# Kernel tuning notes

Measured on AMD Instinct MI355X. Metric: run time of the kernel, lower is better.

Reference implementation:

```python
import jax, jax.numpy as jnp
import numpy as np

TOP_P = 0.9
NEG_FILL = -1000000000.0


def _top_p_mask(logits):
    # probabilities over vocab
    probs = jax.nn.softmax(logits, axis=-1)
    # sort descending; keep the permutation to scatter the mask back
    order = jnp.argsort(-probs, axis=-1)                      # [B, V]
    ordered = jnp.take_along_axis(probs, order, axis=-1)      # [B, V]
    cum = jnp.cumsum(ordered, axis=-1)
    cum = cum.at[..., -1].set(0.0)
    cum = jnp.roll(cum, shift=1, axis=-1)                     # exclusive cumsum
    cmask = cum <= TOP_P                                      # [B, V] in sorted order
    # scatter back: selection[b, order[b, j]] = cmask[b, j]  <=>  gather by inverse perm
    inv = jnp.argsort(order, axis=-1)
    return jnp.take_along_axis(cmask, inv, axis=-1)


def setup_inputs() -> dict:
    key = jax.random.key(0)
    k1, k2 = jax.random.split(key)
    B, V = 256, 128000
    logits = jax.random.normal(k1, (B, V), dtype=jnp.float32)
    u = jax.random.uniform(k2, (B,), dtype=jnp.float32)
    return {"logits": logits, "u": u, "temperature": 1}


def reference(logits, u, temperature):
    t = jnp.asarray(temperature, dtype=logits.dtype)
    logits = logits / t
    sel = _top_p_mask(logits)
    masked = jnp.where(sel, logits, jnp.asarray(NEG_FILL, logits.dtype))
    probs = jax.nn.softmax(masked, axis=-1)                   # [B, V]
    # multinomial(num_samples=1) via inverse-CDF with uniform u
    cdf = jnp.cumsum(probs, axis=-1)
    token = jnp.sum(cdf < u[:, None], axis=-1)
    return jnp.minimum(token, probs.shape[-1] - 1)
```

## Files before the change

### kernel.cpp

```cpp
#include <hip/hip_runtime.h>

#define BLOCK 1024
#define NW (BLOCK / 64)
#define FPSCALE 8192.0f
#define INVSCALE 0x1p-13f

__device__ __forceinline__ float wincl(float v, int lane) {
#pragma unroll
    for (int o = 1; o < 64; o <<= 1) {
        float x = __shfl_up(v, o, 64);
        if (lane >= o) v += x;
    }
    return v;
}

__device__ __forceinline__ void find_crit_desc(const float* h, int n, int seg,
                                               float limit, int lane, int* out_b) {
    float segsum = 0.f;
    int start = n - 1 - lane * seg;
    for (int k = 0; k < seg; k++) segsum += h[start - k];
    float incl = wincl(segsum, lane);
    unsigned long long mk = __ballot(incl > limit);
    if (mk == 0ULL) { *out_b = 0; return; }
    int fl = __ffsll(mk) - 1;
    float base = __shfl(incl, fl, 64) - __shfl(segsum, fl, 64);
    int sstart = n - 1 - fl * seg;
    float v = (lane < seg) ? h[sstart - lane] : 0.f;
    float incl2 = wincl(v, lane);
    unsigned long long mk2 = __ballot((lane < seg) && (base + incl2 > limit));
    int k2 = mk2 ? (__ffsll(mk2) - 1) : (seg - 1);
    *out_b = sstart - k2;
}

#define OKEY(bb) ((bb) ^ ((unsigned)((int)(bb) >> 31) | 0x80000000u))

#define LD4(j) (*(const float4*)(row + (j)))

__global__ __launch_bounds__(BLOCK) void NucleusSampling_79336635892529_kernel(
    const float* __restrict__ logits, const float* __restrict__ uvec,
    const int* __restrict__ temp, int* __restrict__ out, int Vv) {
    const int b = blockIdx.x;
    const float* __restrict__ row = logits + (size_t)b * (size_t)Vv;
    const int t = threadIdx.x;
    const int lane = t & 63;
    const int wave = t >> 6;
    const int rep = lane & 3;

    __shared__ __align__(16) unsigned histbuf[8192];
    __shared__ float mg[2048];
    __shared__ float sweep[NW];
    __shared__ float csum[128];
    __shared__ int shb1;

    const float inv_t = 1.0f / (float)temp[0];
    const int V4 = Vv & ~3;
    const int S = BLOCK * 4;
    const int nch = (Vv + 1023) >> 10;

    for (int i = t; i < 8192; i += BLOCK) histbuf[i] = 0u;
    __syncthreads();

#define P1(xx) { unsigned kk = OKEY(__float_as_uint(xx)); \
                 float e = __expf((xx) * inv_t); \
                 atomicAdd(&histbuf[((kk >> 21) << 2) | rep], \
                           (unsigned)(e * FPSCALE + 0.5f)); }
    {
        int i = t * 4;
        for (; i + 3 * S + 3 < V4; i += 4 * S) {
            float4 a = LD4(i), b4 = LD4(i + S), c = LD4(i + 2 * S), d = LD4(i + 3 * S);
            P1(a.x); P1(a.y); P1(a.z); P1(a.w);
            P1(b4.x); P1(b4.y); P1(b4.z); P1(b4.w);
            P1(c.x); P1(c.y); P1(c.z); P1(c.w);
            P1(d.x); P1(d.y); P1(d.z); P1(d.w);
        }
        for (; i < V4; i += S) { float4 a = LD4(i); P1(a.x); P1(a.y); P1(a.z); P1(a.w); }
        for (int j = V4 + t; j < Vv; j += BLOCK) P1(row[j]);
    }
    __syncthreads();

    float zp = 0.f;
    for (int i = t; i < 2048; i += BLOCK) {
        uint4 m4 = *(const uint4*)&histbuf[i << 2];
        float m = (float)(m4.x + m4.y + m4.z + m4.w) * INVSCALE;
        mg[i] = m;
        zp += m;
    }
#pragma unroll
    for (int o = 32; o >= 1; o >>= 1) zp += __shfl_xor(zp, o, 64);
    if (lane == 0) sweep[wave] = zp;
    __syncthreads();
    float Z = 0.f;
    for (int w = 0; w < NW; w++) Z += sweep[w];
    const float limit = 0.9f * Z;

    if (wave == 0) {
        int b1w;
        find_crit_desc(mg, 2048, 32, limit, lane, &b1w);
        if (lane == 0) shb1 = b1w;
    }
    if (t < 128 && t >= nch) csum[t] = 0.f;
    __syncthreads();
    const unsigned Tlow = (unsigned)shb1 << 21;

#define P2(xx, ss) { unsigned kk = OKEY(__float_as_uint(xx)); \
                     float e = __expf((xx) * inv_t); \
                     if (kk >= Tlow) ss += e; }
    for (int c0 = wave; c0 < nch; c0 += 2 * NW) {
        const int c1 = c0 + NW;
        const bool haveB = (c1 < nch);
        float s0 = 0.f, s1 = 0.f;
        const int bA = c0 << 10, bB = c1 << 10;
        if (bA + 1024 <= Vv && (!haveB || bB + 1024 <= Vv)) {
            float4 a0 = LD4(bA + lane * 4);
            float4 a1 = LD4(bA + 256 + lane * 4);
            float4 a2 = LD4(bA + 512 + lane * 4);
            float4 a3 = LD4(bA + 768 + lane * 4);
            if (haveB) {
                float4 b0 = LD4(bB + lane * 4);
                float4 b1v = LD4(bB + 256 + lane * 4);
                float4 b2 = LD4(bB + 512 + lane * 4);
                float4 b3 = LD4(bB + 768 + lane * 4);
                P2(b0.x, s1); P2(b0.y, s1); P2(b0.z, s1); P2(b0.w, s1);
                P2(b1v.x, s1); P2(b1v.y, s1); P2(b1v.z, s1); P2(b1v.w, s1);
                P2(b2.x, s1); P2(b2.y, s1); P2(b2.z, s1); P2(b2.w, s1);
                P2(b3.x, s1); P2(b3.y, s1); P2(b3.z, s1); P2(b3.w, s1);
            }
            P2(a0.x, s0); P2(a0.y, s0); P2(a0.z, s0); P2(a0.w, s0);
            P2(a1.x, s0); P2(a1.y, s0); P2(a1.z, s0); P2(a1.w, s0);
            P2(a2.x, s0); P2(a2.y, s0); P2(a2.z, s0); P2(a2.w, s0);
            P2(a3.x, s0); P2(a3.y, s0); P2(a3.z, s0); P2(a3.w, s0);
        } else {
            for (int q = 0; q < 16; q++) {
                int i = bA + (q << 6) + lane;
                if (i < Vv) { float x = row[i]; P2(x, s0); }
            }
            if (haveB) {
                for (int q = 0; q < 16; q++) {
                    int i = bB + (q << 6) + lane;
                    if (i < Vv) { float x = row[i]; P2(x, s1); }
                }
            }
        }
#pragma unroll
        for (int o = 32; o >= 1; o >>= 1) s0 += __shfl_xor(s0, o, 64);
        if (lane == 0) csum[c0] = s0;
        if (haveB) {
#pragma unroll
            for (int o = 32; o >= 1; o >>= 1) s1 += __shfl_xor(s1, o, 64);
            if (lane == 0) csum[c1] = s1;
        }
    }
    __syncthreads();

    if (wave == 0) {
        float segsum = csum[lane * 2] + csum[lane * 2 + 1];
        float incl = wincl(segsum, lane);
        float total = __shfl(incl, 63, 64);
        const float U = uvec[b] * total;
        unsigned long long mk = __ballot(incl >= U);
        int token;
        if (mk == 0ULL) {
            token = Vv;
        } else {
            int fl = __ffsll(mk) - 1;
            float base = __shfl(incl, fl, 64) - __shfl(segsum, fl, 64);
            float v = (lane < 2) ? csum[fl * 2 + lane] : 0.f;
            float incl2 = wincl(v, lane);
            unsigned long long mk2 = __ballot((lane < 2) && (base + incl2 >= U));
            int k2i = mk2 ? (__ffsll(mk2) - 1) : 1;
            int cx = fl * 2 + k2i;
            float B = base + __shfl(incl2, k2i, 64) - __shfl(v, k2i, 64);
            int cb = cx << 10;
            float vv[16];
#pragma unroll
            for (int r = 0; r < 16; r++) {
                int idx = cb + r * 64 + lane;
                vv[r] = (idx < Vv) ? row[idx] : -1e30f;
            }
            int cnt2 = 0;
#pragma unroll
            for (int r = 0; r < 16; r++) {
                int idx = cb + r * 64 + lane;
                unsigned kk = OKEY(__float_as_uint(vv[r]));
                float e = __expf(vv[r] * inv_t);
                float keep = (kk >= Tlow) ? e : 0.f;
                float is = wincl(keep, lane);
                unsigned long long mm = __ballot((idx < Vv) && (B + is < U));
                cnt2 += __popcll(mm);
                B += __shfl(is, 63, 64);
            }
            token = cb + cnt2;
        }
        if (lane == 0) out[b] = (token < Vv - 1) ? token : (Vv - 1);
    }
}

extern "C" void kernel_launch(void* const* d_in, const int* in_sizes, int n_in,
                              void* d_out, int out_size, void* d_ws, size_t ws_size,
                              hipStream_t stream) {
    const float* logits = (const float*)d_in[0];
    const float* u = (const float*)d_in[1];
    const int* temp = (const int*)d_in[2];
    int* out = (int*)d_out;
    int B = in_sizes[1];
    int V = in_sizes[0] / B;
    NucleusSampling_79336635892529_kernel<<<B, BLOCK, 0, stream>>>(logits, u, temp, out, V);
}
```

Measured before the change: 213.0 us.

## Split per-row sampling into four kernels with two blocks per row

Replaces the single fused one-block-per-row kernel with four kernels: a histogram pass that uses two blocks per row, a threshold walk, a chunk-sum pass that also uses two blocks per row, and a single-wave pick kernel. Intermediates go through the workspace. With 256 rows, the fused kernel launches only 256 blocks, and the split doubles block count to fill more of the GPU. The cost is extra launches and global-memory round trips for the partial histograms and chunk sums. If the workspace is missing or too small, the original fused kernel still runs.

```diff
diff --git a/kernel.cpp b/kernel.cpp
--- a/kernel.cpp
+++ b/kernel.cpp
@@ -36,6 +36,211 @@
 
 #define LD4(j) (*(const float4*)(row + (j)))
 
+#define P1(xx) { unsigned kk = OKEY(__float_as_uint(xx)); \
+                 float e = __expf((xx) * inv_t); \
+                 atomicAdd(&histbuf[((kk >> 21) << 2) | rep], \
+                           (unsigned)(e * FPSCALE + 0.5f)); }
+
+#define P2(xx, ss) { unsigned kk = OKEY(__float_as_uint(xx)); \
+                     float e = __expf((xx) * inv_t); \
+                     if (kk >= Tlow) ss += e; }
+
+__global__ __launch_bounds__(BLOCK, 8) void ns_hist(
+    const float* __restrict__ logits, const int* __restrict__ temp,
+    unsigned* __restrict__ part, int Vv) {
+    const int bid = blockIdx.x;
+    const int b = bid >> 1, h = bid & 1;
+    const float* __restrict__ row = logits + (size_t)b * (size_t)Vv;
+    const int t = threadIdx.x;
+    const int rep = t & 3;
+
+    __shared__ __align__(16) unsigned histbuf[8192];
+
+    const float inv_t = 1.0f / (float)temp[0];
+    const int S = BLOCK * 4;
+    const int HL = (((Vv + 1) >> 1) + 3) & ~3;
+    const int lo = h * HL;
+    const int hi = min(Vv, lo + HL);
+    const int hi4 = (hi > lo) ? lo + ((hi - lo) & ~3) : lo;
+
+    for (int i = t; i < 8192; i += BLOCK) histbuf[i] = 0u;
+    __syncthreads();
+
+    {
+        int i = lo + t * 4;
+        for (; i + 3 * S + 3 < hi4; i += 4 * S) {
+            float4 a = LD4(i), b4 = LD4(i + S), c = LD4(i + 2 * S), d = LD4(i + 3 * S);
+            P1(a.x); P1(a.y); P1(a.z); P1(a.w);
+            P1(b4.x); P1(b4.y); P1(b4.z); P1(b4.w);
+            P1(c.x); P1(c.y); P1(c.z); P1(c.w);
+            P1(d.x); P1(d.y); P1(d.z); P1(d.w);
+        }
+        for (; i + 3 < hi4; i += S) { float4 a = LD4(i); P1(a.x); P1(a.y); P1(a.z); P1(a.w); }
+        for (int j = hi4 + t; j < hi; j += BLOCK) P1(row[j]);
+    }
+    __syncthreads();
+
+    unsigned* __restrict__ dst = part + (size_t)bid * 2048;
+    for (int i = t; i < 2048; i += BLOCK) {
+        uint4 m4 = *(const uint4*)&histbuf[i << 2];
+        dst[i] = m4.x + m4.y + m4.z + m4.w;
+    }
+}
+
+__global__ __launch_bounds__(BLOCK) void ns_walk(
+    const unsigned* __restrict__ part, unsigned* __restrict__ tlow, int Bn) {
+    const int b = blockIdx.x;
+    const int t = threadIdx.x;
+    const int lane = t & 63;
+    const int wave = t >> 6;
+
+    __shared__ float mg[2048];
+    __shared__ float sweep[NW];
+
+    const unsigned* __restrict__ pa = part + (size_t)(b * 2) * 2048;
+    const unsigned* __restrict__ pb = part + (size_t)(b * 2 + 1) * 2048;
+
+    float zp = 0.f;
+    for (int i = t; i < 2048; i += BLOCK) {
+        float m = (float)(pa[i] + pb[i]) * INVSCALE;
+        mg[i] = m;
+        zp += m;
+    }
+#pragma unroll
+    for (int o = 32; o >= 1; o >>= 1) zp += __shfl_xor(zp, o, 64);
+    if (lane == 0) sweep[wave] = zp;
+    __syncthreads();
+    float Z = 0.f;
+    for (int w = 0; w < NW; w++) Z += sweep[w];
+    const float limit = 0.9f * Z;
+
+    if (wave == 0) {
+        int b1w;
+        find_crit_desc(mg, 2048, 32, limit, lane, &b1w);
+        if (lane == 0) tlow[b] = (unsigned)b1w << 21;
+    }
+}
+
+__global__ __launch_bounds__(BLOCK, 8) void ns_csum(
+    const float* __restrict__ logits, const int* __restrict__ temp,
+    const unsigned* __restrict__ tlow, float* __restrict__ csum, int Vv) {
+    const int bid = blockIdx.x;
+    const int b = bid >> 1, h = bid & 1;
+    const float* __restrict__ row = logits + (size_t)b * (size_t)Vv;
+    const int t = threadIdx.x;
+    const int lane = t & 63;
+    const int wave = t >> 6;
+
+    const float inv_t = 1.0f / (float)temp[0];
+    const unsigned Tlow = tlow[b];
+    const int nch = (Vv + 1023) >> 10;
+    const int nchh = (nch + 1) >> 1;
+    const int clo = h * nchh;
+    const int chi = min(nch, clo + nchh);
+    float* __restrict__ cs = csum + (size_t)b * 128;
+
+    for (int c0 = clo + wave; c0 < chi; c0 += 2 * NW) {
+        const int c1 = c0 + NW;
+        const bool haveB = (c1 < chi);
+        float s0 = 0.f, s1 = 0.f;
+        const int bA = c0 << 10, bB = c1 << 10;
+        if (bA + 1024 <= Vv && (!haveB || bB + 1024 <= Vv)) {
+            float4 a0 = LD4(bA + lane * 4);
+            float4 a1 = LD4(bA + 256 + lane * 4);
+            float4 a2 = LD4(bA + 512 + lane * 4);
+            float4 a3 = LD4(bA + 768 + lane * 4);
+            if (haveB) {
+                float4 b0 = LD4(bB + lane * 4);
+                float4 b1v = LD4(bB + 256 + lane * 4);
+                float4 b2 = LD4(bB + 512 + lane * 4);
+                float4 b3 = LD4(bB + 768 + lane * 4);
+                P2(b0.x, s1); P2(b0.y, s1); P2(b0.z, s1); P2(b0.w, s1);
+                P2(b1v.x, s1); P2(b1v.y, s1); P2(b1v.z, s1); P2(b1v.w, s1);
+                P2(b2.x, s1); P2(b2.y, s1); P2(b2.z, s1); P2(b2.w, s1);
+                P2(b3.x, s1); P2(b3.y, s1); P2(b3.z, s1); P2(b3.w, s1);
+            }
+            P2(a0.x, s0); P2(a0.y, s0); P2(a0.z, s0); P2(a0.w, s0);
+            P2(a1.x, s0); P2(a1.y, s0); P2(a1.z, s0); P2(a1.w, s0);
+            P2(a2.x, s0); P2(a2.y, s0); P2(a2.z, s0); P2(a2.w, s0);
+            P2(a3.x, s0); P2(a3.y, s0); P2(a3.z, s0); P2(a3.w, s0);
+        } else {
+            for (int q = 0; q < 16; q++) {
+                int i = bA + (q << 6) + lane;
+                if (i < Vv) { float x = row[i]; P2(x, s0); }
+            }
+            if (haveB) {
+                for (int q = 0; q < 16; q++) {
+                    int i = bB + (q << 6) + lane;
+                    if (i < Vv) { float x = row[i]; P2(x, s1); }
+                }
+            }
+        }
+#pragma unroll
+        for (int o = 32; o >= 1; o >>= 1) s0 += __shfl_xor(s0, o, 64);
+        if (lane == 0) cs[c0] = s0;
+        if (haveB) {
+#pragma unroll
+            for (int o = 32; o >= 1; o >>= 1) s1 += __shfl_xor(s1, o, 64);
+            if (lane == 0) cs[c1] = s1;
+        }
+    }
+}
+
+__global__ __launch_bounds__(64) void ns_pick(
+    const float* __restrict__ logits, const float* __restrict__ uvec,
+    const int* __restrict__ temp, const unsigned* __restrict__ tlow,
+    const float* __restrict__ csum, int* __restrict__ out, int Vv) {
+    const int b = blockIdx.x;
+    const float* __restrict__ row = logits + (size_t)b * (size_t)Vv;
+    const int lane = threadIdx.x;
+    const float inv_t = 1.0f / (float)temp[0];
+    const unsigned Tlow = tlow[b];
+    const int nch = (Vv + 1023) >> 10;
+    const float* __restrict__ cs = csum + (size_t)b * 128;
+
+    float c0v = (2 * lane < nch) ? cs[2 * lane] : 0.f;
+    float c1v = (2 * lane + 1 < nch) ? cs[2 * lane + 1] : 0.f;
+    float segsum = c0v + c1v;
+    float incl = wincl(segsum, lane);
+    float total = __shfl(incl, 63, 64);
+    const float U = uvec[b] * total;
+    unsigned long long mk = __ballot(incl >= U);
+    int token;
+    if (mk == 0ULL) {
+        token = Vv;
+    } else {
+        int fl = __ffsll(mk) - 1;
+        float base = __shfl(incl, fl, 64) - __shfl(segsum, fl, 64);
+        float v = (lane < 2 && fl * 2 + lane < nch) ? cs[fl * 2 + lane] : 0.f;
+        float incl2 = wincl(v, lane);
+        unsigned long long mk2 = __ballot((lane < 2) && (base + incl2 >= U));
+        int k2i = mk2 ? (__ffsll(mk2) - 1) : 1;
+        int cx = fl * 2 + k2i;
+        float B = base + __shfl(incl2, k2i, 64) - __shfl(v, k2i, 64);
+        int cb = cx << 10;
+        float vv[16];
+#pragma unroll
+        for (int r = 0; r < 16; r++) {
+            int idx = cb + r * 64 + lane;
+            vv[r] = (idx < Vv) ? row[idx] : -1e30f;
+        }
+        int cnt2 = 0;
+#pragma unroll
+        for (int r = 0; r < 16; r++) {
+            int idx = cb + r * 64 + lane;
+            unsigned kk = OKEY(__float_as_uint(vv[r]));
+            float e = __expf(vv[r] * inv_t);
+            float keep = (kk >= Tlow) ? e : 0.f;
+            float is = wincl(keep, lane);
+            unsigned long long mm = __ballot((idx < Vv) && (B + is < U));
+            cnt2 += __popcll(mm);
+            B += __shfl(is, 63, 64);
+        }
+        token = cb + cnt2;
+    }
+    if (lane == 0) out[b] = (token < Vv - 1) ? token : (Vv - 1);
+}
+
 __global__ __launch_bounds__(BLOCK) void NucleusSampling_79336635892529_kernel(
     const float* __restrict__ logits, const float* __restrict__ uvec,
     const int* __restrict__ temp, int* __restrict__ out, int Vv) {
@@ -59,11 +264,6 @@
 
     for (int i = t; i < 8192; i += BLOCK) histbuf[i] = 0u;
     __syncthreads();
-
-#define P1(xx) { unsigned kk = OKEY(__float_as_uint(xx)); \
-                 float e = __expf((xx) * inv_t); \
-                 atomicAdd(&histbuf[((kk >> 21) << 2) | rep], \
-                           (unsigned)(e * FPSCALE + 0.5f)); }
     {
         int i = t * 4;
         for (; i + 3 * S + 3 < V4; i += 4 * S) {
@@ -77,7 +277,6 @@
         for (int j = V4 + t; j < Vv; j += BLOCK) P1(row[j]);
     }
     __syncthreads();
-
     float zp = 0.f;
     for (int i = t; i < 2048; i += BLOCK) {
         uint4 m4 = *(const uint4*)&histbuf[i << 2];
@@ -92,7 +291,6 @@
     float Z = 0.f;
     for (int w = 0; w < NW; w++) Z += sweep[w];
     const float limit = 0.9f * Z;
-
     if (wave == 0) {
         int b1w;
         find_crit_desc(mg, 2048, 32, limit, lane, &b1w);
@@ -102,9 +300,6 @@
     __syncthreads();
     const unsigned Tlow = (unsigned)shb1 << 21;
 
-#define P2(xx, ss) { unsigned kk = OKEY(__float_as_uint(xx)); \
-                     float e = __expf((xx) * inv_t); \
-                     if (kk >= Tlow) ss += e; }
     for (int c0 = wave; c0 < nch; c0 += 2 * NW) {
         const int c1 = c0 + NW;
         const bool haveB = (c1 < nch);
@@ -204,5 +399,23 @@
     int* out = (int*)d_out;
     int B = in_sizes[1];
     int V = in_sizes[0] / B;
-    NucleusSampling_79336635892529_kernel<<<B, BLOCK, 0, stream>>>(logits, u, temp, out, V);
-}
+
+    size_t sz_hist = (size_t)B * 2 * 2048 * sizeof(unsigned);
+    size_t off_tlow = sz_hist;
+    size_t sz_tlow = ((size_t)B * sizeof(unsigned) + 255) & ~(size_t)255;
+    size_t off_csum = off_tlow + sz_tlow;
+    size_t need = off_csum + (size_t)B * 128 * sizeof(float);
+
+    if (d_ws != nullptr && ws_size >= need) {
+        unsigned* part = (unsigned*)d_ws;
+        unsigned* tlow = (unsigned*)((char*)d_ws + off_tlow);
+        float* csum = (float*)((char*)d_ws + off_csum);
+        ns_hist<<<2 * B, BLOCK, 0, stream>>>(logits, temp, part, V);
+        ns_walk<<<B, BLOCK, 0, stream>>>(part, tlow, B);
+        ns_csum<<<2 * B, BLOCK, 0, stream>>>(logits, temp, tlow, csum, V);
+        ns_pick<<<B, 64, 0, stream>>>(logits, u, temp, tlow, csum, out, V);
+    } else {
+        NucleusSampling_79336635892529_kernel<<<B, BLOCK, 0, stream>>>(
+            logits, u, temp, out, V);
+    }
+}
```

Result: slower. 222.6 us (+4.5%).
